# Optimization experiments

Measured on AMD Instinct MI355X. Metric: run time of the kernel, lower is better.

The kernel has to match this reference:

```python
import jax, jax.numpy as jnp
import numpy as np

B, T, D, H, F = 256, 128, 64, 512, 256


def setup_inputs() -> dict:
    key = jax.random.key(0)
    ks = jax.random.split(key, 4)
    return {
        "observations": jax.random.normal(ks[0], (B, T, D), dtype=jnp.float32),
        "Wx": jax.random.normal(ks[1], (D, 4 * H), dtype=jnp.float32) / np.sqrt(D),
        "Wh": jax.random.normal(ks[2], (H, 4 * H), dtype=jnp.float32) / np.sqrt(H),
        "b": jnp.zeros((4 * H,), dtype=jnp.float32),
        "Wd": jax.random.normal(ks[3], (H, F), dtype=jnp.float32) / np.sqrt(H),
        "bd": jnp.zeros((F,), dtype=jnp.float32),
    }


def reference(observations, Wx, Wh, b, Wd, bd):
    # observations: [B, T, D]. Flax nnx.LSTMCell gate order: i, f, g, o;
    # input kernels have no bias, hidden kernels carry the bias.
    batch = observations.shape[0]
    hidden = Wh.shape[0]
    # Precompute input projections for all timesteps in one big GEMM: [T, B, 4H]
    x_proj = jnp.einsum("btd,dg->tbg", observations, Wx)

    def step(carry, xp_t):
        c, h = carry
        gates = xp_t + h @ Wh + b  # [B, 4H]
        i, f, g, o = jnp.split(gates, 4, axis=-1)
        i = jax.nn.sigmoid(i)
        f = jax.nn.sigmoid(f)
        g = jnp.tanh(g)
        o = jax.nn.sigmoid(o)
        c_new = f * c + i * g
        h_new = o * jnp.tanh(c_new)
        return (c_new, h_new), None

    c0 = jnp.zeros((batch, hidden), dtype=observations.dtype)
    h0 = jnp.zeros((batch, hidden), dtype=observations.dtype)
    (c_last, h_last), _ = jax.lax.scan(step, (c0, h0), x_proj)
    return jax.nn.relu(h_last @ Wd + bd)
```

## Files before the change

kernel.cpp:

```cpp
#include <hip/hip_runtime.h>


#define WH_S 524
#define WX_S 72
#define HT_S 524

typedef __attribute__((ext_vector_type(4))) _Float16 f16x4;
typedef __attribute__((ext_vector_type(4))) float    f32x4;
typedef __attribute__((ext_vector_type(4))) unsigned u32x4;
typedef __attribute__((ext_vector_type(2))) unsigned u32x2;

__device__ __forceinline__ float sigm(float x)  { return 1.f / (1.f + __expf(-x)); }
__device__ __forceinline__ float tanh_(float x) { float e = __expf(2.f * x); return 1.f - 2.f / (e + 1.f); }

__device__ __forceinline__ u32x4 ldx4_cc(const unsigned* p) {
    u32x4 v;
    asm volatile("global_load_dwordx4 %0, %1, off sc0 sc1" : "=v"(v) : "v"(p));
    return v;
}
__device__ __forceinline__ void stx4_cc(unsigned* p, u32x4 v) {
    asm volatile("global_store_dwordx4 %0, %1, off sc0 sc1" :: "v"(p), "v"(v) : "memory");
}

#define MFMA16(w, a, c) __builtin_amdgcn_mfma_f32_16x16x16f16((w), (a), (c), 0, 0, 0)

__launch_bounds__(256, 1)
__global__ void lstm_persist(const float* __restrict__ obs,
                             const float* __restrict__ Wx,
                             const float* __restrict__ Wh,
                             const float* __restrict__ bvec,
                             unsigned* __restrict__ hb)
{
    __shared__ _Float16 sbuf[128 * WH_S];

    const int tid = threadIdx.x, lane = tid & 63, wid = tid >> 6;
    const int grp = blockIdx.x & 15, slc = blockIdx.x >> 4;
    const int l15 = lane & 15, l16 = lane >> 4;
    const int c0 = (wid << 5) + l15, c1 = c0 + 16;

    for (int idx = tid; idx < 512 * 128; idx += 256) {
        int k = idx >> 7, c = idx & 127;
        int u = ((c >> 5) << 3) | (c & 7);
        int g = (((c >> 4) & 1) << 1) | ((c >> 3) & 1);
        sbuf[c * WH_S + k] = (_Float16)Wh[k * 2048 + (g << 9) + (slc << 5) + u];
    }
    __syncthreads();
    f16x4 wf0[32], wf1[32];
    #pragma unroll
    for (int kk = 0; kk < 32; ++kk) {
        wf0[kk] = *(const f16x4*)&sbuf[c0 * WH_S + (kk << 4) + (l16 << 2)];
        wf1[kk] = *(const f16x4*)&sbuf[c1 * WH_S + (kk << 4) + (l16 << 2)];
    }
    __syncthreads();
    for (int idx = tid; idx < 64 * 128; idx += 256) {
        int k = idx >> 7, c = idx & 127;
        int u = ((c >> 5) << 3) | (c & 7);
        int g = (((c >> 4) & 1) << 1) | ((c >> 3) & 1);
        sbuf[c * WX_S + k] = (_Float16)Wx[k * 2048 + (g << 9) + (slc << 5) + u];
    }
    __syncthreads();
    f16x4 xw0[4], xw1[4];
    #pragma unroll
    for (int kx = 0; kx < 4; ++kx) {
        xw0[kx] = *(const f16x4*)&sbuf[c0 * WX_S + (kx << 4) + (l16 << 2)];
        xw1[kx] = *(const f16x4*)&sbuf[c1 * WX_S + (kx << 4) + (l16 << 2)];
    }
    __syncthreads();
    _Float16* const sh = sbuf;

    const int brow = (grp << 4) + l15;
    const int ub   = (wid << 3) + ((l16 & 1) << 2);
    f32x4 bia[4];
    #pragma unroll
    for (int g = 0; g < 4; ++g)
        bia[g] = *(const f32x4*)(bvec + (g << 9) + (slc << 5) + ub);

    const int r_ld = (wid << 2) + l16;
    const int ch16 = l15;
    const int rowg = (grp << 4) + r_ld;

    float c_reg[4] = {0.f, 0.f, 0.f, 0.f};

    for (int t = 0; t < 128; ++t) {
        f16x4 xf[4];
        const float* op = obs + ((brow << 7) + t) * 64;
        #pragma unroll
        for (int kx = 0; kx < 4; ++kx) {
            f32x4 ov = *(const f32x4*)(op + (kx << 4) + (l16 << 2));
            #pragma unroll
            for (int e = 0; e < 4; ++e) xf[kx][e] = (_Float16)ov[e];
        }
        __builtin_amdgcn_sched_barrier(0);

        const unsigned tagt = (unsigned)t;
        const unsigned* src = hb + ((t & 1) ? 131072 : 0) + rowg * 512 + (ch16 << 2);
        u32x4 v[8];
        #pragma unroll
        for (int j = 0; j < 8; ++j) v[j] = ldx4_cc(src + (j << 6));
        unsigned pend = 0xffu;
        for (;;) {
            asm volatile("s_waitcnt vmcnt(0)" ::: "memory");
            unsigned np = 0;
            #pragma unroll
            for (int j = 0; j < 8; ++j) {
                if (pend & (1u << j)) {
                    bool ok = ((v[j][0] & 0xffffu) == tagt) & ((v[j][1] & 0xffffu) == tagt)
                            & ((v[j][2] & 0xffffu) == tagt) & ((v[j][3] & 0xffffu) == tagt);
                    if (!ok) { np |= (1u << j); v[j] = ldx4_cc(src + (j << 6)); }
                }
            }
            pend = np;
            if (!__any((int)pend)) break;
        }
        __builtin_amdgcn_sched_barrier(0);

        #pragma unroll
        for (int j = 0; j < 8; ++j) {
            u32x2 wv;
            wv[0] = __builtin_amdgcn_perm(v[j][1], v[j][0], 0x07060302);
            wv[1] = __builtin_amdgcn_perm(v[j][3], v[j][2], 0x07060302);
            *(u32x2*)&sh[r_ld * HT_S + (j << 6) + (ch16 << 2)] = wv;
        }
        __syncthreads();

        f32x4 a00 = {0.f,0.f,0.f,0.f}, a01 = {0.f,0.f,0.f,0.f};
        f32x4 a10 = {0.f,0.f,0.f,0.f}, a11 = {0.f,0.f,0.f,0.f};
        #pragma unroll
        for (int kx = 0; kx < 4; ++kx) {
            if (kx & 1) { a01 = MFMA16(xw0[kx], xf[kx], a01); a11 = MFMA16(xw1[kx], xf[kx], a11); }
            else        { a00 = MFMA16(xw0[kx], xf[kx], a00); a10 = MFMA16(xw1[kx], xf[kx], a10); }
        }
        #pragma unroll
        for (int kk = 0; kk < 32; ++kk) {
            f16x4 af = *(const f16x4*)&sh[l15 * HT_S + (kk << 4) + (l16 << 2)];
            if (kk & 1) { a01 = MFMA16(wf0[kk], af, a01); a11 = MFMA16(wf1[kk], af, a11); }
            else        { a00 = MFMA16(wf0[kk], af, a00); a10 = MFMA16(wf1[kk], af, a10); }
        }
        f32x4 t0 = a00 + a01, t1 = a10 + a11;

        f32x4 r0, r1;
        #pragma unroll
        for (int rr = 0; rr < 4; ++rr) {
            r0[rr] = __shfl_xor(t0[rr], 32, 64);
            r1[rr] = __shfl_xor(t1[rr], 32, 64);
        }
        const bool low = (l16 < 2);
        f16x4 hv;
        #pragma unroll
        for (int rr = 0; rr < 4; ++rr) {
            float I  = low ? t0[rr] : r0[rr];
            float Fv = low ? r0[rr] : t0[rr];
            float G  = low ? t1[rr] : r1[rr];
            float O  = low ? r1[rr] : t1[rr];
            I  = sigm (I  + bia[0][rr]);
            Fv = sigm (Fv + bia[1][rr]);
            G  = tanh_(G  + bia[2][rr]);
            O  = sigm (O  + bia[3][rr]);
            float cn  = Fv * c_reg[rr] + I * G;
            c_reg[rr] = cn;
            hv[rr] = (_Float16)(O * tanh_(cn));
        }
        if (low) {
            unsigned* dst = hb + (((t + 1) & 1) ? 131072 : 0)
                          + (brow << 9) + (slc << 5) + (wid << 3) + ((l16 & 1) << 2);
            u32x4 st;
            #pragma unroll
            for (int rr = 0; rr < 4; ++rr) {
                unsigned short hbits = __builtin_bit_cast(unsigned short, (_Float16)hv[rr]);
                st[rr] = (unsigned)(t + 1) | ((unsigned)hbits << 16);
            }
            stx4_cc(dst, st);
        }
        __syncthreads();
    }
}

__launch_bounds__(256)
__global__ void final_proj(const unsigned* __restrict__ hlast,
                           const float* __restrict__ Wd,
                           const float* __restrict__ bd,
                           float* __restrict__ out)
{
    __shared__ float shm[2048];
    const int tid = threadIdx.x;
    const int rb  = blockIdx.x;
    for (int idx = tid; idx < 2048; idx += 256) {
        unsigned r = hlast[(rb << 2) * 512 + idx];
        shm[idx] = (float)__builtin_bit_cast(_Float16, (unsigned short)(r >> 16));
    }
    __syncthreads();
    float a0 = 0.f, a1 = 0.f, a2 = 0.f, a3 = 0.f;
    for (int k = 0; k < 512; ++k) {
        float w = Wd[(k << 8) + tid];
        a0 += shm[k] * w; a1 += shm[512 + k] * w; a2 += shm[1024 + k] * w; a3 += shm[1536 + k] * w;
    }
    float bb = bd[tid];
    float v0 = a0 + bb, v1 = a1 + bb, v2 = a2 + bb, v3 = a3 + bb;
    out[((rb << 2) + 0) * 256 + tid] = v0 > 0.f ? v0 : 0.f;
    out[((rb << 2) + 1) * 256 + tid] = v1 > 0.f ? v1 : 0.f;
    out[((rb << 2) + 2) * 256 + tid] = v2 > 0.f ? v2 : 0.f;
    out[((rb << 2) + 3) * 256 + tid] = v3 > 0.f ? v3 : 0.f;
}

extern "C" void kernel_launch(void* const* d_in, const int* in_sizes, int n_in,
                              void* d_out, int out_size, void* d_ws, size_t ws_size,
                              hipStream_t stream)
{
    (void)in_sizes; (void)n_in; (void)out_size; (void)ws_size;
    const float* obs = (const float*)d_in[0];
    const float* Wx  = (const float*)d_in[1];
    const float* Wh  = (const float*)d_in[2];
    const float* bv  = (const float*)d_in[3];
    const float* Wd  = (const float*)d_in[4];
    const float* bd  = (const float*)d_in[5];
    float* out = (float*)d_out;

    unsigned* hb = (unsigned*)d_ws;

    hipMemsetAsync(d_ws, 0, 1048576, stream);

    void* args[5];
    args[0] = (void*)&obs; args[1] = (void*)&Wx; args[2] = (void*)&Wh;
    args[3] = (void*)&bv;  args[4] = (void*)&hb;
    hipError_t e = hipLaunchCooperativeKernel((const void*)lstm_persist,
                                              dim3(256), dim3(256), args, 0, stream);
    if (e != hipSuccess) {
        lstm_persist<<<dim3(256), dim3(256), 0, stream>>>(obs, Wx, Wh, bv, hb);
    }
    final_proj<<<dim3(64), dim3(256), 0, stream>>>(hb, Wd, bd, out);
}
```

Before: 643.9 us.

## Add per-group step flags so blocks poll one counter before loading hidden state

Adds a per-group flag array in which each slice block publishes its completed timestep after a block barrier. Wave 0 polls the 16 flags with sleeps before the block reloads h, replacing the polling of tagged hidden-state loads from every wave. The observation loads are now issued after the h loads so they overlap. The existing tag check is kept as a safety net. This adds a flag store, an extra barrier and one more global round trip per step, and it relies on ordering between the h store and the flag store.

Result: faster. 626.2 us (-2.7%).

```diff
diff --git a/kernel.cpp b/kernel.cpp
--- a/kernel.cpp
+++ b/kernel.cpp
@@ -9,6 +9,7 @@
 typedef __attribute__((ext_vector_type(4))) float    f32x4;
 typedef __attribute__((ext_vector_type(4))) unsigned u32x4;
 typedef __attribute__((ext_vector_type(2))) unsigned u32x2;
+typedef unsigned long long u64;
 
 __device__ __forceinline__ float sigm(float x)  { return 1.f / (1.f + __expf(-x)); }
 __device__ __forceinline__ float tanh_(float x) { float e = __expf(2.f * x); return 1.f - 2.f / (e + 1.f); }
@@ -20,6 +21,20 @@
 }
 __device__ __forceinline__ void stx4_cc(unsigned* p, u32x4 v) {
     asm volatile("global_store_dwordx4 %0, %1, off sc0 sc1" :: "v"(p), "v"(v) : "memory");
+}
+__device__ __forceinline__ f32x4 ld128_pl(const void* p) {
+    f32x4 v;
+    asm volatile("global_load_dwordx4 %0, %1, off" : "=v"(v) : "v"(p));
+    return v;
+}
+__device__ __forceinline__ unsigned ldflag_cc(const unsigned* p) {
+    unsigned v;
+    asm volatile("global_load_dword %0, %1, off sc0 sc1\n\ts_waitcnt vmcnt(0)"
+                 : "=v"(v) : "v"(p) : "memory");
+    return v;
+}
+__device__ __forceinline__ void stflag_cc(unsigned* p, unsigned v) {
+    asm volatile("global_store_dword %0, %1, off sc0 sc1" :: "v"(p), "v"(v) : "memory");
 }
 
 #define MFMA16(w, a, c) __builtin_amdgcn_mfma_f32_16x16x16f16((w), (a), (c), 0, 0, 0)
@@ -29,7 +44,8 @@
                              const float* __restrict__ Wx,
                              const float* __restrict__ Wh,
                              const float* __restrict__ bvec,
-                             unsigned* __restrict__ hb)
+                             unsigned* __restrict__ hb,
+                             unsigned* __restrict__ flg)
 {
     __shared__ _Float16 sbuf[128 * WH_S];
 
@@ -78,41 +94,58 @@
     const int r_ld = (wid << 2) + l16;
     const int ch16 = l15;
     const int rowg = (grp << 4) + r_ld;
+    const int hst  = (brow << 9) + (slc << 5) + (wid << 3) + ((l16 & 1) << 2);
+    unsigned* const gflg = flg + (grp << 4);
 
     float c_reg[4] = {0.f, 0.f, 0.f, 0.f};
 
     for (int t = 0; t < 128; ++t) {
-        f16x4 xf[4];
-        const float* op = obs + ((brow << 7) + t) * 64;
-        #pragma unroll
-        for (int kx = 0; kx < 4; ++kx) {
-            f32x4 ov = *(const f32x4*)(op + (kx << 4) + (l16 << 2));
-            #pragma unroll
-            for (int e = 0; e < 4; ++e) xf[kx][e] = (_Float16)ov[e];
-        }
-        __builtin_amdgcn_sched_barrier(0);
-
-        const unsigned tagt = (unsigned)t;
-        const unsigned* src = hb + ((t & 1) ? 131072 : 0) + rowg * 512 + (ch16 << 2);
-        u32x4 v[8];
-        #pragma unroll
-        for (int j = 0; j < 8; ++j) v[j] = ldx4_cc(src + (j << 6));
-        unsigned pend = 0xffu;
-        for (;;) {
-            asm volatile("s_waitcnt vmcnt(0)" ::: "memory");
-            unsigned np = 0;
-            #pragma unroll
-            for (int j = 0; j < 8; ++j) {
-                if (pend & (1u << j)) {
-                    bool ok = ((v[j][0] & 0xffffu) == tagt) & ((v[j][1] & 0xffffu) == tagt)
-                            & ((v[j][2] & 0xffffu) == tagt) & ((v[j][3] & 0xffffu) == tagt);
-                    if (!ok) { np |= (1u << j); v[j] = ldx4_cc(src + (j << 6)); }
+        if (t) {
+            if (wid == 0) {
+                const unsigned tgt = (unsigned)t;
+                for (;;) {
+                    unsigned f = ldflag_cc(gflg + l15);
+                    if (__all((int)(f >= tgt))) break;
+                    __builtin_amdgcn_s_sleep(1);
                 }
             }
-            pend = np;
-            if (!__any((int)pend)) break;
-        }
-        __builtin_amdgcn_sched_barrier(0);
+            __syncthreads();
+        }
+
+        const unsigned* src = hb + ((t & 1) ? 131072 : 0) + (rowg << 9) + (ch16 << 2);
+        u32x4 v[8];
+        #pragma unroll
+        for (int j = 0; j < 8; ++j) v[j] = ldx4_cc(src + (j << 6));
+        f32x4 ov[4];
+        const float* op = obs + ((brow << 7) + t) * 64;
+        #pragma unroll
+        for (int kx = 0; kx < 4; ++kx) ov[kx] = ld128_pl(op + (kx << 4) + (l16 << 2));
+
+        {
+            const unsigned tagt = (unsigned)t;
+            unsigned pend = 0xffu;
+            for (;;) {
+                asm volatile("s_waitcnt vmcnt(0)" ::: "memory");
+                unsigned np = 0;
+                #pragma unroll
+                for (int j = 0; j < 8; ++j) {
+                    if (pend & (1u << j)) {
+                        bool ok = ((v[j][0] & 0xffffu) == tagt) & ((v[j][1] & 0xffffu) == tagt)
+                                & ((v[j][2] & 0xffffu) == tagt) & ((v[j][3] & 0xffffu) == tagt);
+                        if (!ok) { np |= (1u << j); v[j] = ldx4_cc(src + (j << 6)); }
+                    }
+                }
+                pend = np;
+                if (!__any((int)pend)) break;
+            }
+        }
+
+        f16x4 xf[4];
+        #pragma unroll
+        for (int kx = 0; kx < 4; ++kx) {
+            #pragma unroll
+            for (int e = 0; e < 4; ++e) xf[kx][e] = (_Float16)ov[kx][e];
+        }
 
         #pragma unroll
         for (int j = 0; j < 8; ++j) {
@@ -161,8 +194,7 @@
             hv[rr] = (_Float16)(O * tanh_(cn));
         }
         if (low) {
-            unsigned* dst = hb + (((t + 1) & 1) ? 131072 : 0)
-                          + (brow << 9) + (slc << 5) + (wid << 3) + ((l16 & 1) << 2);
+            unsigned* dst = hb + (((t + 1) & 1) ? 131072 : 0) + hst;
             u32x4 st;
             #pragma unroll
             for (int rr = 0; rr < 4; ++rr) {
@@ -171,7 +203,12 @@
             }
             stx4_cc(dst, st);
         }
-        __syncthreads();
+
+        if (t < 127) {
+            __builtin_amdgcn_s_barrier();
+            if (tid == 0)
+                stflag_cc(gflg + slc, (unsigned)(t + 1));
+        }
     }
 }
 
@@ -215,17 +252,18 @@
     const float* bd  = (const float*)d_in[5];
     float* out = (float*)d_out;
 
-    unsigned* hb = (unsigned*)d_ws;
-
-    hipMemsetAsync(d_ws, 0, 1048576, stream);
-
-    void* args[5];
+    unsigned* hb  = (unsigned*)d_ws;
+    unsigned* flg = (unsigned*)((char*)d_ws + 1048576);
+
+    (void)hipMemsetAsync(d_ws, 0, 1048576 + 1024, stream);
+
+    void* args[6];
     args[0] = (void*)&obs; args[1] = (void*)&Wx; args[2] = (void*)&Wh;
-    args[3] = (void*)&bv;  args[4] = (void*)&hb;
+    args[3] = (void*)&bv;  args[4] = (void*)&hb; args[5] = (void*)&flg;
     hipError_t e = hipLaunchCooperativeKernel((const void*)lstm_persist,
                                               dim3(256), dim3(256), args, 0, stream);
     if (e != hipSuccess) {
-        lstm_persist<<<dim3(256), dim3(256), 0, stream>>>(obs, Wx, Wh, bv, hb);
+        lstm_persist<<<dim3(256), dim3(256), 0, stream>>>(obs, Wx, Wh, bv, hb, flg);
     }
     final_proj<<<dim3(64), dim3(256), 0, stream>>>(hb, Wd, bd, out);
 }
```
